# Optimization experiments

Hardware: AMD Instinct MI355X
Metric: run time of the kernel (lower is better)

## Reference

```python
import jax, jax.numpy as jnp
import numpy as np

N, E, B, D, H, C = 50000, 800000, 128, 64, 128, 2
EPS = 1e-5


def setup_inputs() -> dict:
    key = jax.random.key(0)
    ks = jax.random.split(key, 12)
    s = 0.1
    return {
        "x": jax.random.normal(ks[0], (N, D), jnp.float32),
        "edge_index": jax.random.randint(ks[1], (2, E), 0, N, jnp.int64),
        "batch": jnp.sort(jax.random.randint(ks[2], (N,), 0, B, jnp.int64)),
        "W_l": jax.random.normal(ks[3], (D, D), jnp.float32) * s,
        "b_l": jnp.zeros((D,), jnp.float32),
        "W_r": jax.random.normal(ks[4], (D, D), jnp.float32) * s,
        "W_res": jax.random.normal(ks[5], (D, D), jnp.float32) * s,
        "b_res": jnp.zeros((D,), jnp.float32),
        "gamma": jnp.ones((D,), jnp.float32),
        "beta": jnp.zeros((D,), jnp.float32),
        "gate_W1": jax.random.normal(ks[6], (D, D), jnp.float32) * s,
        "gate_b1": jnp.zeros((D,), jnp.float32),
        "gate_W2": jax.random.normal(ks[7], (D, 1), jnp.float32) * s,
        "gate_b2": jnp.zeros((1,), jnp.float32),
        "W_p1": jax.random.normal(ks[8], (D, H), jnp.float32) * s,
        "b_p1": jnp.zeros((H,), jnp.float32),
        "W_p2": jax.random.normal(ks[9], (H, C), jnp.float32) * s,
        "b_p2": jnp.zeros((C,), jnp.float32),
    }


def reference(x, edge_index, batch, W_l, b_l, W_r, W_res, b_res, gamma, beta,
              gate_W1, gate_b1, gate_W2, gate_b2, W_p1, b_p1, W_p2, b_p2):
    src, dst = edge_index[0], edge_index[1]
    # SAGEConv, mean aggregation: gather source feats, scatter-mean to target
    agg = jax.ops.segment_sum(x[src], dst, num_segments=N)          # [N, D]
    cnt = jax.ops.segment_sum(jnp.ones((E,), x.dtype), dst, num_segments=N)
    mean = agg / jnp.maximum(cnt, 1.0)[:, None]
    h = mean @ W_l + b_l + x @ W_r                                   # [N, D]
    # dropout is identity (eval mode)
    # BatchNorm1d (training-mode math: biased batch stats)
    mu = jnp.mean(h, axis=0)
    var = jnp.var(h, axis=0)
    h = (h - mu) * jax.lax.rsqrt(var + EPS) * gamma + beta
    # residual projection of the original features
    h = h + x @ W_res + b_res
    # GlobalAttention pooling: per-graph softmax over gate scores
    gate = jax.nn.relu(h @ gate_W1 + gate_b1) @ gate_W2 + gate_b2    # [N, 1]
    g = gate[:, 0]
    gmax = jax.ops.segment_max(g, batch, num_segments=B)
    gmax = jnp.where(jnp.isfinite(gmax), gmax, 0.0)
    e = jnp.exp(g - gmax[batch])
    z = jax.ops.segment_sum(e, batch, num_segments=B)
    alpha = e / jnp.maximum(z, 1e-16)[batch]
    pooled = jax.ops.segment_sum(alpha[:, None] * h, batch, num_segments=B)  # [B, D]
    # 2-layer predictor MLP with ReLU between
    out = jax.nn.relu(pooled @ W_p1 + b_p1) @ W_p2 + b_p2            # [B, C]
    return out
```

## Files before the change

kernel.cpp:

```cpp
#include <hip/hip_runtime.h>
#include <math.h>

#define N_NODES 50000
#define N_EDGES 800000
#define BATCHES 128
#define DIM 64
#define HID 128
#define NCLS 2
#define EPSV 1e-5f
#define MAXD 64

#define NBLK 782
#define EPB  1024

#define MREP 4
#define MSTRIDE 32
#define BAR_STRIDE 512

typedef __attribute__((ext_vector_type(8))) short bf16x8;
typedef __attribute__((ext_vector_type(4))) float f32x4;

__device__ __forceinline__ unsigned short f2bf(float f){
  unsigned u = __float_as_uint(f);
  u += 0x7FFFu + ((u >> 16) & 1u);
  return (unsigned short)(u >> 16);
}
__device__ __forceinline__ float bf2f(unsigned short h){
  return __uint_as_float(((unsigned)h) << 16);
}
__device__ __forceinline__ void split2(float f, unsigned short& hi, unsigned short& lo){
  hi = f2bf(f);
  lo = f2bf(f - bf2f(hi));
}
__device__ __forceinline__ uint4 pack8(const unsigned short* s){
  uint4 u;
  u.x = (unsigned)s[0] | ((unsigned)s[1] << 16);
  u.y = (unsigned)s[2] | ((unsigned)s[3] << 16);
  u.z = (unsigned)s[4] | ((unsigned)s[5] << 16);
  u.w = (unsigned)s[6] | ((unsigned)s[7] << 16);
  return u;
}

__device__ __forceinline__ float gload(const float* p){
  return __hip_atomic_load(p, __ATOMIC_RELAXED, __HIP_MEMORY_SCOPE_AGENT);
}
__device__ __forceinline__ int iload(const int* p){
  return __hip_atomic_load(p, __ATOMIC_RELAXED, __HIP_MEMORY_SCOPE_AGENT);
}
__device__ __forceinline__ unsigned uload(const unsigned* p){
  return __hip_atomic_load(p, __ATOMIC_RELAXED, __HIP_MEMORY_SCOPE_AGENT);
}
__device__ __forceinline__ void ustore(unsigned* p, unsigned v){
  __hip_atomic_store(p, v, __ATOMIC_RELAXED, __HIP_MEMORY_SCOPE_AGENT);
}

__device__ __forceinline__ void gbar(unsigned* bb, int bx){
  __syncthreads();
  if (threadIdx.x == 0){
    const int k = bx & 7;
    const unsigned quota = (k < (NBLK & 7)) ? (unsigned)(NBLK/8 + 1)
                                            : (unsigned)(NBLK/8);
    unsigned old = __hip_atomic_fetch_add(&bb[k*32], 1u,
                     __ATOMIC_RELAXED, __HIP_MEMORY_SCOPE_AGENT);
    if (old == quota - 1u){
      unsigned r = __hip_atomic_fetch_add(&bb[8*32], 1u,
                     __ATOMIC_RELAXED, __HIP_MEMORY_SCOPE_AGENT);
      if (r == 7u)
        __hip_atomic_store(&bb[9*32], 1u,
                     __ATOMIC_RELAXED, __HIP_MEMORY_SCOPE_AGENT);
    }
    while (__hip_atomic_load(&bb[9*32],
                     __ATOMIC_RELAXED, __HIP_MEMORY_SCOPE_AGENT) == 0u)
      __builtin_amdgcn_s_sleep(32);
  }
  asm volatile("" ::: "memory");
  __syncthreads();
}

__device__ __forceinline__ void stage_w64(short* sWh, short* sWl_,
                                          const float* __restrict__ W,
                                          int w, int lane){
  const int k0 = 16 * w;
  #pragma unroll
  for (int kc = 0; kc < 2; ++kc){
    unsigned short h[8], l[8];
    #pragma unroll
    for (int i = 0; i < 8; ++i){
      int k = k0 + 8*kc + i;
      split2(W[k*DIM + lane], h[i], l[i]);
    }
    *(uint4*)&sWh[lane*72 + k0 + 8*kc] = pack8(h);
    *(uint4*)&sWl_[lane*72 + k0 + 8*kc] = pack8(l);
  }
}

#define GEMM64(ACC) do { \
  _Pragma("unroll") \
  for (int kt2 = 0; kt2 < 2; ++kt2){ \
    const int ka = kt2*32 + koff; \
    bf16x8 ah = *(const bf16x8*)&sA[0][mrow][ka]; \
    bf16x8 al = *(const bf16x8*)&sA[1][mrow][ka]; \
    _Pragma("unroll") \
    for (int nt = 0; nt < 4; ++nt){ \
      const int nr = nt*16 + jc; \
      bf16x8 bh = *(const bf16x8*)&sB[0][nr][ka]; \
      bf16x8 bo = *(const bf16x8*)&sB[1][nr][ka]; \
      ACC[nt] = __builtin_amdgcn_mfma_f32_16x16x32_bf16(ah, bh, ACC[nt], 0,0,0); \
      ACC[nt] = __builtin_amdgcn_mfma_f32_16x16x32_bf16(al, bh, ACC[nt], 0,0,0); \
      ACC[nt] = __builtin_amdgcn_mfma_f32_16x16x32_bf16(ah, bo, ACC[nt], 0,0,0); \
    } \
  } \
} while(0)

#define STAGE_A(SRC) do { \
  const int row_  = tid >> 2; \
  const int kq_   = (tid & 3) * 16; \
  const int node_ = base + row_; \
  _Pragma("unroll") \
  for (int cc = 0; cc < 4; ++cc){ \
    float4 v = make_float4(0.f,0.f,0.f,0.f); \
    if (node_ < N_NODES) v = *(const float4*)&SRC[(size_t)node_*DIM + kq_ + 4*cc]; \
    unsigned short h_[4], l_[4]; \
    split2(v.x,h_[0],l_[0]); split2(v.y,h_[1],l_[1]); \
    split2(v.z,h_[2],l_[2]); split2(v.w,h_[3],l_[3]); \
    uint2 ph_, pl_; \
    ph_.x = (unsigned)h_[0] | ((unsigned)h_[1]<<16); \
    ph_.y = (unsigned)h_[2] | ((unsigned)h_[3]<<16); \
    pl_.x = (unsigned)l_[0] | ((unsigned)l_[1]<<16); \
    pl_.y = (unsigned)l_[2] | ((unsigned)l_[3]<<16); \
    *(uint2*)&sA[0][row_][kq_ + 4*cc] = ph_; \
    *(uint2*)&sA[1][row_][kq_ + 4*cc] = pl_; \
  } \
} while(0)

__global__ void __launch_bounds__(256, 4) k_mega(
    const int* __restrict__ ei, const float* __restrict__ x,
    const float* __restrict__ Wl, const float* __restrict__ bl,
    const float* __restrict__ Wr,
    const float* __restrict__ Wres, const float* __restrict__ bres,
    const float* __restrict__ gamma, const float* __restrict__ beta,
    const float* __restrict__ gW1, const float* __restrict__ gb1,
    const float* __restrict__ gW2, const float* __restrict__ gb2,
    const float* __restrict__ Wp1, const float* __restrict__ bp1,
    const float* __restrict__ Wp2, const float* __restrict__ bp2,
    const int* __restrict__ batch,
    int* __restrict__ cnt, unsigned* __restrict__ csr32,
    float* __restrict__ musum,
    float* __restrict__ zbuf, float* __restrict__ pooled,
    unsigned* __restrict__ bar, float* __restrict__ outp){
  __shared__ __align__(16) short sA[2][64][72];
  __shared__ __align__(16) short sB[2][64][72];
  __shared__ int sb[64];
  __shared__ unsigned long long runmask;
  __shared__ float smu[2*DIM];
  __shared__ float psh[DIM];
  __shared__ float redh[4];

  const int tid  = threadIdx.x;
  const int lane = tid & 63, w = tid >> 6;
  const int jc   = lane & 15;
  const int g16  = w*4 + (lane >> 4);
  const int mrow = 16*w + jc;
  const int koff = (lane >> 4) * 8;
  const int r0   = 16*w + (lane >> 4)*4;
  const int bx   = blockIdx.x;
  const int base = bx * 64;

  {
    const int e0 = bx * EPB + tid;
    #pragma unroll
    for (int q = 0; q < 4; ++q){
      const int i = e0 + q*256;
      if (i < N_EDGES){
        int d = ei[N_EDGES + i];
        int s = ei[i];
        int pos = atomicAdd(&cnt[d], 1);
        ustore(&csr32[(size_t)pos*N_NODES + d], (unsigned)s);
      }
    }
  }
  gbar(bar, bx);

  {
    float* sBf = (float*)&sB[0][0][0];
    const int g = lane >> 4, f = lane & 15;
    for (int n16 = 0; n16 < 16; ++n16){
      const int row = w*16 + n16;
      const int node = base + row;
      const int dg = (node < N_NODES) ? iload(&cnt[node]) : 0;
      float4 a4 = make_float4(0.f,0.f,0.f,0.f);
      int e = 0;
      if (lane < dg) e = (int)uload(&csr32[(size_t)lane*N_NODES + node]);
      int i = 0;
      for (; i + 16 <= dg; i += 16){
        int s0 = __shfl(e, i +      g, 64);
        int s1 = __shfl(e, i + 4  + g, 64);
        int s2 = __shfl(e, i + 8  + g, 64);
        int s3 = __shfl(e, i + 12 + g, 64);
        float4 v0 = *(const float4*)&x[(size_t)s0*DIM + f*4];
        float4 v1 = *(const float4*)&x[(size_t)s1*DIM + f*4];
        float4 v2 = *(const float4*)&x[(size_t)s2*DIM + f*4];
        float4 v3 = *(const float4*)&x[(size_t)s3*DIM + f*4];
        a4.x += v0.x + v1.x + v2.x + v3.x;
        a4.y += v0.y + v1.y + v2.y + v3.y;
        a4.z += v0.z + v1.z + v2.z + v3.z;
        a4.w += v0.w + v1.w + v2.w + v3.w;
      }
      for (; i < dg; i += 4){
        int idx = i + g;
        int srcl = (idx < dg) ? idx : (dg - 1);
        int s = __shfl(e, srcl, 64);
        if (idx < dg){
          float4 v = *(const float4*)&x[(size_t)s*DIM + f*4];
          a4.x += v.x; a4.y += v.y; a4.z += v.z; a4.w += v.w;
        }
      }
      a4.x += __shfl_xor(a4.x, 16, 64); a4.x += __shfl_xor(a4.x, 32, 64);
      a4.y += __shfl_xor(a4.y, 16, 64); a4.y += __shfl_xor(a4.y, 32, 64);
      a4.z += __shfl_xor(a4.z, 16, 64); a4.z += __shfl_xor(a4.z, 32, 64);
      a4.w += __shfl_xor(a4.w, 16, 64); a4.w += __shfl_xor(a4.w, 32, 64);
      if (g == 0){
        float inv = 1.f / fmaxf((float)dg, 1.f);
        *(float4*)&sBf[row*64 + 4*f] =
          make_float4(a4.x*inv, a4.y*inv, a4.z*inv, a4.w*inv);
      }
    }
  }
  __syncthreads();

  float blv[4];
  #pragma unroll
  for (int nt = 0; nt < 4; ++nt) blv[nt] = bl[nt*16 + jc];

  f32x4 acc[4] = {};
  {
    float* sBf = (float*)&sB[0][0][0];
    const int row_ = tid >> 2;
    const int kq_  = (tid & 3) * 16;
    float4 mv[4];
    #pragma unroll
    for (int cc = 0; cc < 4; ++cc)
      mv[cc] = *(float4*)&sBf[row_*64 + kq_ + 4*cc];
    __syncthreads();
    #pragma unroll
    for (int cc = 0; cc < 4; ++cc){
      unsigned short h_[4], l_[4];
      split2(mv[cc].x,h_[0],l_[0]); split2(mv[cc].y,h_[1],l_[1]);
      split2(mv[cc].z,h_[2],l_[2]); split2(mv[cc].w,h_[3],l_[3]);
      uint2 ph_, pl_;
      ph_.x = (unsigned)h_[0] | ((unsigned)h_[1]<<16);
      ph_.y = (unsigned)h_[2] | ((unsigned)h_[3]<<16);
      pl_.x = (unsigned)l_[0] | ((unsigned)l_[1]<<16);
      pl_.y = (unsigned)l_[2] | ((unsigned)l_[3]<<16);
      *(uint2*)&sA[0][row_][kq_ + 4*cc] = ph_;
      *(uint2*)&sA[1][row_][kq_ + 4*cc] = pl_;
    }
    stage_w64(&sB[0][0][0], &sB[1][0][0], Wl, w, lane);
  }
  __syncthreads();
  GEMM64(acc);
  __syncthreads();
  stage_w64(&sB[0][0][0], &sB[1][0][0], Wr, w, lane);
  STAGE_A(x);
  __syncthreads();
  GEMM64(acc);

  float s1v[4] = {0.f,0.f,0.f,0.f}, s2v[4] = {0.f,0.f,0.f,0.f};
  #pragma unroll
  for (int nt = 0; nt < 4; ++nt){
    #pragma unroll
    for (int r = 0; r < 4; ++r){
      const int node = base + r0 + r;
      float v = acc[nt][r] + blv[nt];
      acc[nt][r] = v;
      if (node < N_NODES){ s1v[nt] += v; s2v[nt] += v*v; }
    }
  }
  __syncthreads();
  {
    float* sred = (float*)&sB[0][0][0];
    #pragma unroll
    for (int nt = 0; nt < 4; ++nt){
      float a = s1v[nt], b = s2v[nt];
      a += __shfl_xor(a, 16, 64); a += __shfl_xor(a, 32, 64);
      b += __shfl_xor(b, 16, 64); b += __shfl_xor(b, 32, 64);
      if ((lane >> 4) == 0){
        sred[0*256 + w*64 + nt*16 + jc] = a;
        sred[1*256 + w*64 + nt*16 + jc] = b;
      }
    }
    __syncthreads();
    const int rep = bx & (MREP-1);
    if (tid < 64){
      float a = sred[tid] + sred[64+tid] + sred[128+tid] + sred[192+tid];
      float b = sred[256+tid] + sred[320+tid] + sred[384+tid] + sred[448+tid];
      atomicAdd(&musum[(size_t)rep*128*MSTRIDE + (size_t)tid*MSTRIDE], a);
      atomicAdd(&musum[(size_t)rep*128*MSTRIDE + (size_t)(64+tid)*MSTRIDE], b);
    }
  }
  gbar(bar + BAR_STRIDE, bx);

  if (tid < 64){
    float s1 = 0.f, s2 = 0.f;
    #pragma unroll
    for (int rep = 0; rep < MREP; ++rep){
      s1 += gload(&musum[(size_t)rep*128*MSTRIDE + (size_t)tid*MSTRIDE]);
      s2 += gload(&musum[(size_t)rep*128*MSTRIDE + (size_t)(64+tid)*MSTRIDE]);
    }
    float mu = s1 / (float)N_NODES;
    float var = s2 / (float)N_NODES - mu*mu;
    smu[tid] = mu;
    smu[DIM+tid] = 1.0f / sqrtf(var + EPSV);
  }
  if (tid < 64){
    int nn = base + tid;
    sb[tid] = batch[(nn < N_NODES) ? nn : (N_NODES-1)];
  }
  stage_w64(&sB[0][0][0], &sB[1][0][0], Wres, w, lane);
  __syncthreads();

  float muv[4], invv[4], gav[4], bev[4], brv[4], g1v[4], w2v[4];
  #pragma unroll
  for (int nt = 0; nt < 4; ++nt){
    const int col = nt*16 + jc;
    muv[nt] = smu[col];    invv[nt] = smu[DIM+col];
    gav[nt] = gamma[col];  bev[nt]  = beta[col];
    brv[nt] = bres[col];   g1v[nt]  = gb1[col];
    w2v[nt] = gW2[col];
  }
  const float gb2v = gb2[0];
  if (w == 0){
    bool fl = (lane > 0) && (sb[lane] != sb[lane-1]);
    unsigned long long mm = __ballot(fl);
    if (lane == 0) runmask = mm;
  }

  f32x4 acc2[4] = {};
  GEMM64(acc2);

  #pragma unroll
  for (int nt = 0; nt < 4; ++nt){
    const int col = nt*16 + jc;
    #pragma unroll
    for (int r = 0; r < 4; ++r){
      float v = (acc[nt][r] - muv[nt])*invv[nt]*gav[nt] + bev[nt]
              + brv[nt] + acc2[nt][r];
      acc[nt][r] = v;
      unsigned short hh, ll;
      split2(v, hh, ll);
      sA[0][r0 + r][col] = (short)hh;
      sA[1][r0 + r][col] = (short)ll;
    }
  }
  __syncthreads();
  stage_w64(&sB[0][0][0], &sB[1][0][0], gW1, w, lane);
  __syncthreads();

  f32x4 acc3[4] = {};
  GEMM64(acc3);

  float p[4] = {0.f,0.f,0.f,0.f};
  #pragma unroll
  for (int nt = 0; nt < 4; ++nt){
    #pragma unroll
    for (int r = 0; r < 4; ++r)
      p[r] += fmaxf(acc3[nt][r] + g1v[nt], 0.f) * w2v[nt];
  }
  float ev[4];
  #pragma unroll
  for (int r = 0; r < 4; ++r){
    float t = p[r];
    t += __shfl_xor(t, 1, 64); t += __shfl_xor(t, 2, 64);
    t += __shfl_xor(t, 4, 64); t += __shfl_xor(t, 8, 64);
    const int node = base + r0 + r;
    ev[r] = (node < N_NODES) ? expf(t + gb2v) : 0.f;
  }

  {
    float* sredp = (float*)&sA[0][0][0];
    float* szl   = sredp + 16*64;
    __syncthreads();
    const unsigned long long m = runmask;
    int rstart = 0;
    while (rstart < 64){
      const int bseg = sb[rstart];
      unsigned long long rest = (rstart >= 63) ? 0ull : (m >> (rstart+1));
      const int rend = rest ? (rstart + 1 + __builtin_ctzll(rest)) : 64;
      float pacc[4] = {0.f,0.f,0.f,0.f};
      float zacc = 0.f;
      #pragma unroll
      for (int r = 0; r < 4; ++r){
        const int ln = 4*g16 + r;
        if (ln >= rstart && ln < rend){
          #pragma unroll
          for (int nt = 0; nt < 4; ++nt) pacc[nt] += ev[r]*acc[nt][r];
          zacc += ev[r];
        }
      }
      #pragma unroll
      for (int nt = 0; nt < 4; ++nt) sredp[g16*64 + nt*16 + jc] = pacc[nt];
      if ((lane & 15) == 0) szl[g16] = zacc;
      __syncthreads();
      if (tid < 64){
        float s = 0.f;
        for (int g2 = 0; g2 < 16; ++g2) s += sredp[g2*64 + tid];
        atomicAdd(&pooled[bseg*DIM + tid], s);
      }
      if (tid == 64){
        float sz2 = 0.f;
        for (int g2 = 0; g2 < 16; ++g2) sz2 += szl[g2];
        atomicAdd(&zbuf[bseg], sz2);
      }
      __syncthreads();
      rstart = rend;
    }
  }
  gbar(bar + 2*BAR_STRIDE, bx);

  if (bx < BATCHES){
    const int b = bx;
    const int t = tid;
    if (t < DIM){
      float zz = fmaxf(gload(&zbuf[b]), 1e-16f);
      psh[t] = gload(&pooled[b*DIM + t]) / zz;
    }
    __syncthreads();
    if (t < HID){
      float a = bp1[t];
      #pragma unroll
      for (int d2 = 0; d2 < DIM; ++d2) a = fmaf(psh[d2], Wp1[d2*HID + t], a);
      a = fmaxf(a, 0.f);
      float o0 = a * Wp2[t*NCLS+0];
      float o1 = a * Wp2[t*NCLS+1];
      #pragma unroll
      for (int o = 32; o > 0; o >>= 1){
        o0 += __shfl_down(o0, o, 64); o1 += __shfl_down(o1, o, 64);
      }
      int hw = t >> 6;
      if ((t & 63) == 0){ redh[hw*2+0] = o0; redh[hw*2+1] = o1; }
    }
    __syncthreads();
    if (t == 0){
      outp[b*NCLS+0] = redh[0]+redh[2]+bp2[0];
      outp[b*NCLS+1] = redh[1]+redh[3]+bp2[1];
    }
  }
}

extern "C" void kernel_launch(void* const* d_in, const int* in_sizes, int n_in,
                              void* d_out, int out_size, void* d_ws, size_t ws_size,
                              hipStream_t stream){
  const float* x     = (const float*)d_in[0];
  const int*   ei    = (const int*)d_in[1];
  const int*   batch = (const int*)d_in[2];
  const float* Wl    = (const float*)d_in[3];
  const float* bl    = (const float*)d_in[4];
  const float* Wr    = (const float*)d_in[5];
  const float* Wres  = (const float*)d_in[6];
  const float* bres  = (const float*)d_in[7];
  const float* gamma = (const float*)d_in[8];
  const float* beta  = (const float*)d_in[9];
  const float* gW1   = (const float*)d_in[10];
  const float* gb1   = (const float*)d_in[11];
  const float* gW2   = (const float*)d_in[12];
  const float* gb2   = (const float*)d_in[13];
  const float* Wp1   = (const float*)d_in[14];
  const float* bp1   = (const float*)d_in[15];
  const float* Wp2   = (const float*)d_in[16];
  const float* bp2   = (const float*)d_in[17];
  float* outp = (float*)d_out;

  int*      cnt    = (int*)d_ws;
  float*    zbuf   = (float*)(cnt + N_NODES);
  float*    pooled = zbuf + BATCHES;
  unsigned* bar    = (unsigned*)(pooled + (size_t)BATCHES*DIM);
  float*    musum  = (float*)(bar + 3*BAR_STRIDE);
  unsigned* csr32  = (unsigned*)(musum + (size_t)MREP*128*MSTRIDE);

  const size_t zcount = (size_t)N_NODES + BATCHES + (size_t)BATCHES*DIM
                      + 3*BAR_STRIDE + (size_t)MREP*128*MSTRIDE;
  hipMemsetAsync(d_ws, 0, zcount*sizeof(int), stream);

  k_mega<<<NBLK, 256, 0, stream>>>(ei, x, Wl, bl, Wr, Wres, bres,
                                   gamma, beta, gW1, gb1, gW2, gb2,
                                   Wp1, bp1, Wp2, bp2, batch,
                                   cnt, csr32, musum, zbuf, pooled, bar, outp);
}
```

Baseline: 207.7 us.

## Store per-node CSR neighbor lists contiguously and batch edge atomics

New measurement: 203.7 us. About the same (-1.9%).

```diff
diff --git a/kernel.cpp b/kernel.cpp
--- a/kernel.cpp
+++ b/kernel.cpp
@@ -42,12 +42,6 @@
 }
 
 __device__ __forceinline__ float gload(const float* p){
-  return __hip_atomic_load(p, __ATOMIC_RELAXED, __HIP_MEMORY_SCOPE_AGENT);
-}
-__device__ __forceinline__ int iload(const int* p){
-  return __hip_atomic_load(p, __ATOMIC_RELAXED, __HIP_MEMORY_SCOPE_AGENT);
-}
-__device__ __forceinline__ unsigned uload(const unsigned* p){
   return __hip_atomic_load(p, __ATOMIC_RELAXED, __HIP_MEMORY_SCOPE_AGENT);
 }
 __device__ __forceinline__ void ustore(unsigned* p, unsigned v){
@@ -168,16 +162,23 @@
 
   {
     const int e0 = bx * EPB + tid;
-    #pragma unroll
-    for (int q = 0; q < 4; ++q){
-      const int i = e0 + q*256;
-      if (i < N_EDGES){
-        int d = ei[N_EDGES + i];
-        int s = ei[i];
-        int pos = atomicAdd(&cnt[d], 1);
-        ustore(&csr32[(size_t)pos*N_NODES + d], (unsigned)s);
-      }
-    }
+    const int i0 = e0, i1 = e0 + 256, i2 = e0 + 512, i3 = e0 + 768;
+    const bool v0 = i0 < N_EDGES, v1 = i1 < N_EDGES,
+               v2 = i2 < N_EDGES, v3 = i3 < N_EDGES;
+    int d0=0,s0=0,d1=0,s1=0,d2=0,s2=0,d3=0,s3=0;
+    if (v0){ d0 = ei[N_EDGES + i0]; s0 = ei[i0]; }
+    if (v1){ d1 = ei[N_EDGES + i1]; s1 = ei[i1]; }
+    if (v2){ d2 = ei[N_EDGES + i2]; s2 = ei[i2]; }
+    if (v3){ d3 = ei[N_EDGES + i3]; s3 = ei[i3]; }
+    int p0=0,p1=0,p2=0,p3=0;
+    if (v0) p0 = atomicAdd(&cnt[d0], 1);
+    if (v1) p1 = atomicAdd(&cnt[d1], 1);
+    if (v2) p2 = atomicAdd(&cnt[d2], 1);
+    if (v3) p3 = atomicAdd(&cnt[d3], 1);
+    if (v0) ustore(&csr32[(size_t)d0*MAXD + p0], (unsigned)s0);
+    if (v1) ustore(&csr32[(size_t)d1*MAXD + p1], (unsigned)s1);
+    if (v2) ustore(&csr32[(size_t)d2*MAXD + p2], (unsigned)s2);
+    if (v3) ustore(&csr32[(size_t)d3*MAXD + p3], (unsigned)s3);
   }
   gbar(bar, bx);
 
@@ -187,10 +188,10 @@
     for (int n16 = 0; n16 < 16; ++n16){
       const int row = w*16 + n16;
       const int node = base + row;
-      const int dg = (node < N_NODES) ? iload(&cnt[node]) : 0;
+      const int dg = (node < N_NODES) ? cnt[node] : 0;
       float4 a4 = make_float4(0.f,0.f,0.f,0.f);
       int e = 0;
-      if (lane < dg) e = (int)uload(&csr32[(size_t)lane*N_NODES + node]);
+      if (lane < dg) e = (int)csr32[(size_t)node*MAXD + lane];
       int i = 0;
       for (; i + 16 <= dg; i += 16){
         int s0 = __shfl(e, i +      g, 64);
```
